# Kernel tuning notes

Hardware: AMD Instinct MI355X
Metric: run time of the kernel (lower is better)

## Reference

```python
import jax, jax.numpy as jnp
import numpy as np

N, F_IN = 4096, 128
UNITS0, HEADS0 = 16, 4   # hidden GraphAttention layer
UNITS1, HEADS1 = 1, 1    # final layer (sigmoid, mean over last axis)


def _glorot(key, shape):
    fan_in, fan_out = shape[0], shape[1]
    std = (2.0 / (fan_in + fan_out)) ** 0.5
    return std * jax.random.normal(key, shape, dtype=jnp.float32)


def setup_inputs() -> dict:
    key = jax.random.key(0)
    ks = jax.random.split(key, 8)
    x = jax.random.normal(ks[0], (N, F_IN), dtype=jnp.float32)
    adj = (jax.random.uniform(ks[1], (N, N)) < 0.01).astype(jnp.float32)
    return {
        "x": x,
        "adj": adj,
        "w0": _glorot(ks[2], (F_IN, UNITS0)),
        "aw1_0": _glorot(ks[3], (UNITS0, HEADS0)),
        "aw2_0": _glorot(ks[4], (UNITS0, HEADS0)),
        "w1": _glorot(ks[5], (UNITS0 * HEADS0, UNITS1)),
        "aw1_1": _glorot(ks[6], (UNITS1, HEADS1)),
        "aw2_1": _glorot(ks[7], (UNITS1, HEADS1)),
    }


def _gat_layer(x, adj, w, aw1, aw2, activation, final_layer):
    h = x @ w                                   # [N, units]
    a1 = h @ aw1                                # [N, H]
    a2 = h @ aw2                                # [N, H]
    # relu(a1_i + a2_j) broadcast -> [N, N, H]
    coeffs = jax.nn.relu(a1[:, None, :] + a2[None, :, :])
    # elementwise adjacency mask then softmax over neighbor axis (axis=1),
    # matching tf.nn.softmax(adj * coeffs[:,:,i], axis=1)
    attn = jax.nn.softmax(adj[:, :, None] * coeffs, axis=1)   # [N, N, H]
    # per-head aggregation then concat heads: [N, H*units]
    out = jnp.einsum('ijh,jd->ihd', attn, h).reshape(h.shape[0], -1)
    if final_layer:
        out = out.mean(axis=-1)                 # [N]
    return activation(out)


def reference(x, adj, w0, aw1_0, aw2_0, w1, aw1_1, aw2_1):
    h = _gat_layer(x, adj, w0, aw1_0, aw2_0, jax.nn.relu, False)   # [N, 64]
    out = _gat_layer(h, adj, w1, aw1_1, aw2_1, jax.nn.sigmoid, True)  # [N]
    return out
```

## Files before the change

### kernel.cpp

```cpp
#include <hip/hip_runtime.h>
#include <hip/hip_bf16.h>

#define N 4096
#define FIN 128
#define U0 16
#define H0 4
#define MAXD 128
#define NGEMM (N / 16)
#define NCSR4 (N / 4)
#define FSTRIDE 32

__global__ void k1_fused(const float* __restrict__ adj, const float* __restrict__ x,
                         const float* __restrict__ w0, const float* __restrict__ aw1,
                         const float* __restrict__ aw2,
                         int* __restrict__ deg, int* __restrict__ cols,
                         float* __restrict__ F, float* __restrict__ a1,
                         float* __restrict__ S0) {
    const int t = threadIdx.x;
    if (blockIdx.x < NGEMM) {
        const int bid = blockIdx.x;
        __shared__ float xs[16][FIN + 1];
        __shared__ float ws[FIN][U0];
        __shared__ float hs[16][U0 + 1];
        const int r0 = bid * 16;

        for (int k = t; k < FIN * U0; k += 256) ws[k / U0][k % U0] = w0[k];
        for (int k = t; k < 16 * FIN; k += 256)
            xs[k / FIN][k % FIN] = x[(size_t)(r0 + k / FIN) * FIN + (k % FIN)];
        __syncthreads();

        const int r = t / U0, u = t % U0;
        float acc = 0.f;
        #pragma unroll 8
        for (int k = 0; k < FIN; ++k) acc += xs[r][k] * ws[k][u];
        hs[r][u] = acc;
        F[(size_t)(r0 + r) * FSTRIDE + u] = acc;
        __syncthreads();

        if (t < 16 * H0) {
            const int rr = t / H0, hh = t % H0;
            float s1 = 0.f, s2 = 0.f;
            #pragma unroll
            for (int u2 = 0; u2 < U0; ++u2) {
                float hv = hs[rr][u2];
                s1 += hv * aw1[u2 * H0 + hh];
                s2 += hv * aw2[u2 * H0 + hh];
            }
            a1[(r0 + rr) * H0 + hh] = s1;
            F[(size_t)(r0 + rr) * FSTRIDE + 16 + hh] = s2;
        } else if (t >= 128 && t < 144) {
            const int d = t - 128;
            float s = 0.f;
            #pragma unroll
            for (int rr = 0; rr < 16; ++rr) s += hs[rr][d];
            atomicAdd(&S0[d], s);
        }
    } else {
        const int rb4 = (blockIdx.x - NGEMM) * 4;
        const int lane = t & 63, wid = t >> 6;

        __shared__ int cls[2][MAXD];
        __shared__ int wsum[4];
        __shared__ int dgs[2];

        for (int pair = 0; pair < 2; ++pair) {
            const int rb = rb4 + pair * 2;
            const float4* __restrict__ ar0 =
                reinterpret_cast<const float4*>(adj + (size_t)rb * N);
            const float4* __restrict__ ar1 =
                reinterpret_cast<const float4*>(adj + (size_t)(rb + 1) * N);
            float4 v0[4], v1[4];
            #pragma unroll
            for (int p = 0; p < 4; ++p) v0[p] = ar0[t + 256 * p];
            #pragma unroll
            for (int p = 0; p < 4; ++p) v1[p] = ar1[t + 256 * p];

            #pragma unroll
            for (int rr = 0; rr < 2; ++rr) {
                const float4* v = rr ? v1 : v0;
                int c = 0;
                #pragma unroll
                for (int p = 0; p < 4; ++p)
                    c += (v[p].x != 0.f) + (v[p].y != 0.f) + (v[p].z != 0.f) + (v[p].w != 0.f);

                int sc = c;
                #pragma unroll
                for (int s = 1; s < 64; s <<= 1) {
                    int u = __shfl_up(sc, s);
                    if (lane >= s) sc += u;
                }
                if (rr || pair) __syncthreads();
                if (lane == 63) wsum[wid] = sc;
                __syncthreads();
                int base = 0;
                #pragma unroll
                for (int w2 = 0; w2 < 4; ++w2)
                    if (w2 < wid) base += wsum[w2];
                const int off = base + sc - c;
                if (t == 255) dgs[rr] = min(base + sc, MAXD);

                int w = off;
                #pragma unroll
                for (int p = 0; p < 4; ++p) {
                    const int j0 = (t + 256 * p) * 4;
                    if (v[p].x != 0.f && w < MAXD) cls[rr][w++] = j0;
                    if (v[p].y != 0.f && w < MAXD) cls[rr][w++] = j0 + 1;
                    if (v[p].z != 0.f && w < MAXD) cls[rr][w++] = j0 + 2;
                    if (v[p].w != 0.f && w < MAXD) cls[rr][w++] = j0 + 3;
                }
            }
            __syncthreads();
            if (t < dgs[0]) cols[(size_t)rb * MAXD + t] = cls[0][t];
            const int t2 = t - 128;
            if (t2 >= 0 && t2 < dgs[1] && t2 < 128)
                cols[(size_t)(rb + 1) * MAXD + t2] = cls[1][t2];
            if (t < 128) {
                const int k2 = t + 128;
                if (k2 < dgs[1]) cols[(size_t)(rb + 1) * MAXD + k2] = cls[1][k2];
            }
            if (t == 0) { deg[rb] = dgs[0]; deg[rb + 1] = dgs[1]; }
        }
    }
}

__global__ void attn0(const float* __restrict__ F, const float* __restrict__ a1,
                      const float* __restrict__ S0,
                      const int* __restrict__ deg, const int* __restrict__ cols,
                      const float* __restrict__ w1, float* __restrict__ hp) {
    const int i0 = blockIdx.x * 4;
    const int t = threadIdx.x;
    __shared__ int cls[4][MAXD];

    for (int k = t; k < 4 * MAXD; k += 256) {
        const int row = k >> 7, idx = k & 127;
        const int dgr = deg[i0 + row];
        cls[row][idx] = (idx < dgr) ? cols[(size_t)(i0 + row) * MAXD + idx] : 0;
    }
    __syncthreads();

    const int w = t >> 6, lane = t & 63;
    const int i = i0 + w;
    const int dg = deg[i];
    const int q = lane >> 4, r = lane & 15;
    const int hh = r >> 2, dgc = r & 3;
    const float a1v = a1[i * H0 + hh];

    float4 accn = make_float4(0.f, 0.f, 0.f, 0.f);
    float accd = 0.f;
    for (int kb = 0; kb < dg; kb += 8) {
        const int kA = kb + q;
        const int kB = kb + 4 + q;
        const int jA = cls[w][kA < MAXD ? kA : 0];
        const int jB = cls[w][kB < MAXD ? kB : 0];
        const float msA = (kA < dg) ? 1.f : 0.f;
        const float msB = (kB < dg) ? 1.f : 0.f;
        const float* __restrict__ fA = F + (size_t)jA * FSTRIDE;
        const float* __restrict__ fB = F + (size_t)jB * FSTRIDE;
        const float4 hA = *reinterpret_cast<const float4*>(fA + dgc * 4);
        const float a2A = fA[16 + hh];
        const float4 hB = *reinterpret_cast<const float4*>(fB + dgc * 4);
        const float a2B = fB[16 + hh];

        float ccA = a1v + a2A;
        ccA = ccA > 0.f ? ccA : 0.f;
        const float eA = (__expf(ccA) - 1.f) * msA;
        accn.x = fmaf(eA, hA.x, accn.x);
        accn.y = fmaf(eA, hA.y, accn.y);
        accn.z = fmaf(eA, hA.z, accn.z);
        accn.w = fmaf(eA, hA.w, accn.w);
        accd += eA;

        float ccB = a1v + a2B;
        ccB = ccB > 0.f ? ccB : 0.f;
        const float eB = (__expf(ccB) - 1.f) * msB;
        accn.x = fmaf(eB, hB.x, accn.x);
        accn.y = fmaf(eB, hB.y, accn.y);
        accn.z = fmaf(eB, hB.z, accn.z);
        accn.w = fmaf(eB, hB.w, accn.w);
        accd += eB;
    }

    #pragma unroll
    for (int m = 16; m <= 32; m <<= 1) {
        accn.x += __shfl_xor(accn.x, m);
        accn.y += __shfl_xor(accn.y, m);
        accn.z += __shfl_xor(accn.z, m);
        accn.w += __shfl_xor(accn.w, m);
        accd   += __shfl_xor(accd, m);
    }

    const float4 s0v = reinterpret_cast<const float4*>(S0)[dgc];
    const float4 w1v = reinterpret_cast<const float4*>(w1)[r];
    const float inv = 1.f / (accd + (float)N);
    float ox = (accn.x + s0v.x) * inv; ox = ox > 0.f ? ox : 0.f;
    float oy = (accn.y + s0v.y) * inv; oy = oy > 0.f ? oy : 0.f;
    float oz = (accn.z + s0v.z) * inv; oz = oz > 0.f ? oz : 0.f;
    float ow = (accn.w + s0v.w) * inv; ow = ow > 0.f ? ow : 0.f;
    float pv = ox * w1v.x + oy * w1v.y + oz * w1v.z + ow * w1v.w;

    #pragma unroll
    for (int m = 1; m <= 8; m <<= 1) pv += __shfl_xor(pv, m);
    if (lane == 0) hp[i] = pv;
}

__global__ void attn1(const float* __restrict__ hp,
                      const float* __restrict__ aw11, const float* __restrict__ aw21,
                      const int* __restrict__ deg, const int* __restrict__ cols,
                      float* __restrict__ out) {
    __shared__ float hps[N];
    __shared__ int cls[4][MAXD];
    __shared__ float s1red[4];
    const int t = threadIdx.x;
    const int w = t >> 6, lane = t & 63;
    const int i0 = blockIdx.x * 4;

    float s = 0.f;
    const float4* __restrict__ hp4 = reinterpret_cast<const float4*>(hp);
    #pragma unroll
    for (int k = t; k < N / 4; k += 256) {
        float4 v = hp4[k];
        reinterpret_cast<float4*>(hps)[k] = v;
        s += v.x + v.y + v.z + v.w;
    }
    for (int k = t; k < 4 * MAXD; k += 256)
        cls[k >> 7][k & 127] = cols[(size_t)(i0 + (k >> 7)) * MAXD + (k & 127)];

    #pragma unroll
    for (int o = 32; o; o >>= 1) s += __shfl_down(s, o);
    if (lane == 0) s1red[w] = s;
    __syncthreads();
    const float S1 = s1red[0] + s1red[1] + s1red[2] + s1red[3];

    const int i = i0 + w;
    const float w1v = aw11[0], w2v = aw21[0];
    const float a1v = hps[i] * w1v;
    const int dg = deg[i];

    float accn = 0.f, accd = 0.f;
    for (int k = lane; k < dg; k += 64) {
        const int j = cls[w][k];
        const float hj = hps[j];
        float cc = a1v + hj * w2v;
        cc = cc > 0.f ? cc : 0.f;
        const float e = __expf(cc) - 1.f;
        accn = fmaf(e, hj, accn);
        accd += e;
    }
    #pragma unroll
    for (int o = 32; o; o >>= 1) {
        accn += __shfl_down(accn, o);
        accd += __shfl_down(accd, o);
    }
    if (lane == 0) {
        const float v = (accn + S1) / (accd + (float)N);
        out[i] = 1.f / (1.f + __expf(-v));
    }
}

extern "C" void kernel_launch(void* const* d_in, const int* in_sizes, int n_in,
                              void* d_out, int out_size, void* d_ws, size_t ws_size,
                              hipStream_t stream) {
    const float* x    = (const float*)d_in[0];
    const float* adj  = (const float*)d_in[1];
    const float* w0   = (const float*)d_in[2];
    const float* aw10 = (const float*)d_in[3];
    const float* aw20 = (const float*)d_in[4];
    const float* w1   = (const float*)d_in[5];
    const float* aw11 = (const float*)d_in[6];
    const float* aw21 = (const float*)d_in[7];
    float* out = (float*)d_out;

    char* p = (char*)d_ws;
    auto alloc = [&](size_t bytes) {
        char* r = p;
        p += (bytes + 255) & ~(size_t)255;
        return r;
    };
    float* S0   = (float*)alloc(256);
    float* F    = (float*)alloc((size_t)N * FSTRIDE * 4);
    float* a1   = (float*)alloc((size_t)N * H0 * 4);
    float* hp   = (float*)alloc((size_t)N * 4);
    int*   deg  = (int*)alloc((size_t)N * 4);
    int*   cols = (int*)alloc((size_t)N * MAXD * 4);

    hipMemsetAsync(S0, 0, 64, stream);
    k1_fused<<<NGEMM + NCSR4, 256, 0, stream>>>(adj, x, w0, aw10, aw20,
                                                deg, cols, F, a1, S0);
    attn0<<<N / 4, 256, 0, stream>>>(F, a1, S0, deg, cols, w1, hp);
    attn1<<<N / 4, 256, 0, stream>>>(hp, aw11, aw21, deg, cols, out);
}
```

Before: 34.71 us.

## Fuse attention layers into one kernel with a grid-wide flag barrier

Merges the two attention kernels into a single launch. Each block publishes a per-block flag after writing its layer-0 outputs, and every block spins until all 1024 flags are set before running layer 1. This removes one kernel launch and its drain/fill gap. In exchange it depends on all 1024 blocks being co-resident, which launch_bounds(256,4) is meant to allow across the CUs; otherwise it deadlocks. Every block also polls the flag array.

```diff
diff --git a/kernel.cpp b/kernel.cpp
--- a/kernel.cpp
+++ b/kernel.cpp
@@ -8,7 +8,9 @@
 #define MAXD 128
 #define NGEMM (N / 16)
 #define NCSR4 (N / 4)
+#define NATT  (N / 4)
 #define FSTRIDE 32
+#define SCOPE __HIP_MEMORY_SCOPE_AGENT
 
 __global__ void k1_fused(const float* __restrict__ adj, const float* __restrict__ x,
                          const float* __restrict__ w0, const float* __restrict__ aw1,
@@ -123,13 +125,21 @@
     }
 }
 
-__global__ void attn0(const float* __restrict__ F, const float* __restrict__ a1,
-                      const float* __restrict__ S0,
-                      const int* __restrict__ deg, const int* __restrict__ cols,
-                      const float* __restrict__ w1, float* __restrict__ hp) {
-    const int i0 = blockIdx.x * 4;
+__global__ __launch_bounds__(256, 4)
+void attn_mega(const float* __restrict__ F, const float* __restrict__ a1,
+               const float* __restrict__ S0,
+               const int* __restrict__ deg, const int* __restrict__ cols,
+               const float* __restrict__ w1,
+               const float* __restrict__ aw11, const float* __restrict__ aw21,
+               int* __restrict__ flagB, float* __restrict__ hp,
+               float* __restrict__ out) {
+    __shared__ int cls[4][MAXD];
+    __shared__ float hps[N];
+    __shared__ float s1red[4];
+    const int b = blockIdx.x;
+    const int i0 = b * 4;
     const int t = threadIdx.x;
-    __shared__ int cls[4][MAXD];
+    const int w = t >> 6, lane = t & 63;
 
     for (int k = t; k < 4 * MAXD; k += 256) {
         const int row = k >> 7, idx = k & 127;
@@ -138,122 +148,124 @@
     }
     __syncthreads();
 
-    const int w = t >> 6, lane = t & 63;
     const int i = i0 + w;
     const int dg = deg[i];
-    const int q = lane >> 4, r = lane & 15;
-    const int hh = r >> 2, dgc = r & 3;
-    const float a1v = a1[i * H0 + hh];
-
-    float4 accn = make_float4(0.f, 0.f, 0.f, 0.f);
-    float accd = 0.f;
-    for (int kb = 0; kb < dg; kb += 8) {
-        const int kA = kb + q;
-        const int kB = kb + 4 + q;
-        const int jA = cls[w][kA < MAXD ? kA : 0];
-        const int jB = cls[w][kB < MAXD ? kB : 0];
-        const float msA = (kA < dg) ? 1.f : 0.f;
-        const float msB = (kB < dg) ? 1.f : 0.f;
-        const float* __restrict__ fA = F + (size_t)jA * FSTRIDE;
-        const float* __restrict__ fB = F + (size_t)jB * FSTRIDE;
-        const float4 hA = *reinterpret_cast<const float4*>(fA + dgc * 4);
-        const float a2A = fA[16 + hh];
-        const float4 hB = *reinterpret_cast<const float4*>(fB + dgc * 4);
-        const float a2B = fB[16 + hh];
-
-        float ccA = a1v + a2A;
-        ccA = ccA > 0.f ? ccA : 0.f;
-        const float eA = (__expf(ccA) - 1.f) * msA;
-        accn.x = fmaf(eA, hA.x, accn.x);
-        accn.y = fmaf(eA, hA.y, accn.y);
-        accn.z = fmaf(eA, hA.z, accn.z);
-        accn.w = fmaf(eA, hA.w, accn.w);
-        accd += eA;
-
-        float ccB = a1v + a2B;
-        ccB = ccB > 0.f ? ccB : 0.f;
-        const float eB = (__expf(ccB) - 1.f) * msB;
-        accn.x = fmaf(eB, hB.x, accn.x);
-        accn.y = fmaf(eB, hB.y, accn.y);
-        accn.z = fmaf(eB, hB.z, accn.z);
-        accn.w = fmaf(eB, hB.w, accn.w);
-        accd += eB;
-    }
-
-    #pragma unroll
-    for (int m = 16; m <= 32; m <<= 1) {
-        accn.x += __shfl_xor(accn.x, m);
-        accn.y += __shfl_xor(accn.y, m);
-        accn.z += __shfl_xor(accn.z, m);
-        accn.w += __shfl_xor(accn.w, m);
-        accd   += __shfl_xor(accd, m);
-    }
-
-    const float4 s0v = reinterpret_cast<const float4*>(S0)[dgc];
-    const float4 w1v = reinterpret_cast<const float4*>(w1)[r];
-    const float inv = 1.f / (accd + (float)N);
-    float ox = (accn.x + s0v.x) * inv; ox = ox > 0.f ? ox : 0.f;
-    float oy = (accn.y + s0v.y) * inv; oy = oy > 0.f ? oy : 0.f;
-    float oz = (accn.z + s0v.z) * inv; oz = oz > 0.f ? oz : 0.f;
-    float ow = (accn.w + s0v.w) * inv; ow = ow > 0.f ? ow : 0.f;
-    float pv = ox * w1v.x + oy * w1v.y + oz * w1v.z + ow * w1v.w;
-
-    #pragma unroll
-    for (int m = 1; m <= 8; m <<= 1) pv += __shfl_xor(pv, m);
-    if (lane == 0) hp[i] = pv;
-}
-
-__global__ void attn1(const float* __restrict__ hp,
-                      const float* __restrict__ aw11, const float* __restrict__ aw21,
-                      const int* __restrict__ deg, const int* __restrict__ cols,
-                      float* __restrict__ out) {
-    __shared__ float hps[N];
-    __shared__ int cls[4][MAXD];
-    __shared__ float s1red[4];
-    const int t = threadIdx.x;
-    const int w = t >> 6, lane = t & 63;
-    const int i0 = blockIdx.x * 4;
-
-    float s = 0.f;
-    const float4* __restrict__ hp4 = reinterpret_cast<const float4*>(hp);
-    #pragma unroll
-    for (int k = t; k < N / 4; k += 256) {
-        float4 v = hp4[k];
-        reinterpret_cast<float4*>(hps)[k] = v;
-        s += v.x + v.y + v.z + v.w;
-    }
-    for (int k = t; k < 4 * MAXD; k += 256)
-        cls[k >> 7][k & 127] = cols[(size_t)(i0 + (k >> 7)) * MAXD + (k & 127)];
-
-    #pragma unroll
-    for (int o = 32; o; o >>= 1) s += __shfl_down(s, o);
-    if (lane == 0) s1red[w] = s;
+
+    {
+        const int q = lane >> 4, r = lane & 15;
+        const int hh = r >> 2, dgc = r & 3;
+        const float a1v = a1[i * H0 + hh];
+
+        float4 accn = make_float4(0.f, 0.f, 0.f, 0.f);
+        float accd = 0.f;
+        for (int kb = 0; kb < dg; kb += 8) {
+            const int kA = kb + q;
+            const int kB = kb + 4 + q;
+            const int jA = cls[w][kA < MAXD ? kA : 0];
+            const int jB = cls[w][kB < MAXD ? kB : 0];
+            const float msA = (kA < dg) ? 1.f : 0.f;
+            const float msB = (kB < dg) ? 1.f : 0.f;
+            const float* __restrict__ fA = F + (size_t)jA * FSTRIDE;
+            const float* __restrict__ fB = F + (size_t)jB * FSTRIDE;
+            const float4 hA = *reinterpret_cast<const float4*>(fA + dgc * 4);
+            const float a2A = fA[16 + hh];
+            const float4 hB = *reinterpret_cast<const float4*>(fB + dgc * 4);
+            const float a2B = fB[16 + hh];
+
+            float ccA = a1v + a2A;
+            ccA = ccA > 0.f ? ccA : 0.f;
+            const float eA = (__expf(ccA) - 1.f) * msA;
+            accn.x = fmaf(eA, hA.x, accn.x);
+            accn.y = fmaf(eA, hA.y, accn.y);
+            accn.z = fmaf(eA, hA.z, accn.z);
+            accn.w = fmaf(eA, hA.w, accn.w);
+            accd += eA;
+
+            float ccB = a1v + a2B;
+            ccB = ccB > 0.f ? ccB : 0.f;
+            const float eB = (__expf(ccB) - 1.f) * msB;
+            accn.x = fmaf(eB, hB.x, accn.x);
+            accn.y = fmaf(eB, hB.y, accn.y);
+            accn.z = fmaf(eB, hB.z, accn.z);
+            accn.w = fmaf(eB, hB.w, accn.w);
+            accd += eB;
+        }
+        #pragma unroll
+        for (int m = 16; m <= 32; m <<= 1) {
+            accn.x += __shfl_xor(accn.x, m);
+            accn.y += __shfl_xor(accn.y, m);
+            accn.z += __shfl_xor(accn.z, m);
+            accn.w += __shfl_xor(accn.w, m);
+            accd   += __shfl_xor(accd, m);
+        }
+        const float4 s0v = reinterpret_cast<const float4*>(S0)[dgc];
+        const float4 w1v = reinterpret_cast<const float4*>(w1)[r];
+        const float inv = 1.f / (accd + (float)N);
+        float ox = (accn.x + s0v.x) * inv; ox = ox > 0.f ? ox : 0.f;
+        float oy = (accn.y + s0v.y) * inv; oy = oy > 0.f ? oy : 0.f;
+        float oz = (accn.z + s0v.z) * inv; oz = oz > 0.f ? oz : 0.f;
+        float ow = (accn.w + s0v.w) * inv; ow = ow > 0.f ? ow : 0.f;
+        float pv = ox * w1v.x + oy * w1v.y + oz * w1v.z + ow * w1v.w;
+        #pragma unroll
+        for (int m = 1; m <= 8; m <<= 1) pv += __shfl_xor(pv, m);
+        if (lane == 0) hp[i] = pv;
+    }
+
     __syncthreads();
-    const float S1 = s1red[0] + s1red[1] + s1red[2] + s1red[3];
-
-    const int i = i0 + w;
-    const float w1v = aw11[0], w2v = aw21[0];
-    const float a1v = hps[i] * w1v;
-    const int dg = deg[i];
-
-    float accn = 0.f, accd = 0.f;
-    for (int k = lane; k < dg; k += 64) {
-        const int j = cls[w][k];
-        const float hj = hps[j];
-        float cc = a1v + hj * w2v;
-        cc = cc > 0.f ? cc : 0.f;
-        const float e = __expf(cc) - 1.f;
-        accn = fmaf(e, hj, accn);
-        accd += e;
-    }
-    #pragma unroll
-    for (int o = 32; o; o >>= 1) {
-        accn += __shfl_down(accn, o);
-        accd += __shfl_down(accd, o);
-    }
-    if (lane == 0) {
-        const float v = (accn + S1) / (accd + (float)N);
-        out[i] = 1.f / (1.f + __expf(-v));
+    if (t == 0) {
+        __threadfence();
+        __hip_atomic_store(&flagB[b], 1, __ATOMIC_RELEASE, SCOPE);
+    }
+    if (w == 0) {
+        for (;;) {
+            int v = 1;
+            #pragma unroll
+            for (int k = 0; k < 16; ++k)
+                v &= __hip_atomic_load(&flagB[(k << 6) | lane], __ATOMIC_RELAXED, SCOPE);
+            if (__all(v)) break;
+            __builtin_amdgcn_s_sleep(2);
+        }
+    }
+    __syncthreads();
+    if (t == 0) __threadfence();
+    __syncthreads();
+
+    {
+        float s = 0.f;
+        const float4* __restrict__ hp4 = reinterpret_cast<const float4*>(hp);
+        #pragma unroll
+        for (int k = t; k < N / 4; k += 256) {
+            float4 v = hp4[k];
+            reinterpret_cast<float4*>(hps)[k] = v;
+            s += v.x + v.y + v.z + v.w;
+        }
+        #pragma unroll
+        for (int o = 32; o; o >>= 1) s += __shfl_down(s, o);
+        if (lane == 0) s1red[w] = s;
+        __syncthreads();
+        const float S1 = s1red[0] + s1red[1] + s1red[2] + s1red[3];
+
+        const float w1s = aw11[0], w2s = aw21[0];
+        const float a1v1 = hps[i] * w1s;
+        float accn = 0.f, accd = 0.f;
+        for (int k = lane; k < dg; k += 64) {
+            const int j = cls[w][k];
+            const float hj = hps[j];
+            float cc = a1v1 + hj * w2s;
+            cc = cc > 0.f ? cc : 0.f;
+            const float e = __expf(cc) - 1.f;
+            accn = fmaf(e, hj, accn);
+            accd += e;
+        }
+        #pragma unroll
+        for (int o = 32; o; o >>= 1) {
+            accn += __shfl_down(accn, o);
+            accd += __shfl_down(accd, o);
+        }
+        if (lane == 0) {
+            const float v = (accn + S1) / (accd + (float)N);
+            out[i] = 1.f / (1.f + __expf(-v));
+        }
     }
 }
 
@@ -276,16 +288,17 @@
         p += (bytes + 255) & ~(size_t)255;
         return r;
     };
-    float* S0   = (float*)alloc(256);
-    float* F    = (float*)alloc((size_t)N * FSTRIDE * 4);
-    float* a1   = (float*)alloc((size_t)N * H0 * 4);
-    float* hp   = (float*)alloc((size_t)N * 4);
-    int*   deg  = (int*)alloc((size_t)N * 4);
-    int*   cols = (int*)alloc((size_t)N * MAXD * 4);
-
-    hipMemsetAsync(S0, 0, 64, stream);
+    float* S0    = (float*)alloc(256);
+    int*   flagB = (int*)alloc(NATT * 4);
+    float* F     = (float*)alloc((size_t)N * FSTRIDE * 4);
+    float* a1    = (float*)alloc((size_t)N * H0 * 4);
+    float* hp    = (float*)alloc((size_t)N * 4);
+    int*   deg   = (int*)alloc((size_t)N * 4);
+    int*   cols  = (int*)alloc((size_t)N * MAXD * 4);
+
+    hipMemsetAsync(S0, 0, 256 + NATT * 4, stream);
     k1_fused<<<NGEMM + NCSR4, 256, 0, stream>>>(adj, x, w0, aw10, aw20,
                                                 deg, cols, F, a1, S0);
-    attn0<<<N / 4, 256, 0, stream>>>(F, a1, S0, deg, cols, w1, hp);
-    attn1<<<N / 4, 256, 0, stream>>>(hp, aw11, aw21, deg, cols, out);
+    attn_mega<<<NATT, 256, 0, stream>>>(F, a1, S0, deg, cols, w1,
+                                        aw11, aw21, flagB, hp, out);
 }
```

Result: slower. 84.82 us (+144.4%).

## Fuse CSR build into layer-0 attention and replace atomic S0 with partial sums

Applied to the files above, without the earlier changes.

The adjacency-to-CSR compaction moves out of the first kernel and into the layer-0 attention kernel, so each block builds its four rows' neighbor lists in shared memory and uses them directly instead of reloading cols/deg from global memory. The GEMM kernel now writes per-block partial column sums of h, and every attention block reduces the 256 partials itself. This removes the memset and the atomics. The trade-off is that the 64MB adjacency scan now runs after the GEMM instead of alongside it, and each block repeats the S0 reduction.

```diff
diff --git a/kernel.cpp b/kernel.cpp
--- a/kernel.cpp
+++ b/kernel.cpp
@@ -7,140 +7,142 @@
 #define H0 4
 #define MAXD 128
 #define NGEMM (N / 16)
-#define NCSR4 (N / 4)
+#define NATT  (N / 4)
 #define FSTRIDE 32
 
-__global__ void k1_fused(const float* __restrict__ adj, const float* __restrict__ x,
-                         const float* __restrict__ w0, const float* __restrict__ aw1,
-                         const float* __restrict__ aw2,
-                         int* __restrict__ deg, int* __restrict__ cols,
-                         float* __restrict__ F, float* __restrict__ a1,
-                         float* __restrict__ S0) {
+__global__ void k1_gemm(const float* __restrict__ x, const float* __restrict__ w0,
+                        const float* __restrict__ aw1, const float* __restrict__ aw2,
+                        float* __restrict__ F, float* __restrict__ a1,
+                        float* __restrict__ partS0) {
+    __shared__ float xs[16][FIN + 1];
+    __shared__ float ws[FIN][U0];
+    __shared__ float hs[16][U0 + 1];
     const int t = threadIdx.x;
-    if (blockIdx.x < NGEMM) {
-        const int bid = blockIdx.x;
-        __shared__ float xs[16][FIN + 1];
-        __shared__ float ws[FIN][U0];
-        __shared__ float hs[16][U0 + 1];
-        const int r0 = bid * 16;
-
-        for (int k = t; k < FIN * U0; k += 256) ws[k / U0][k % U0] = w0[k];
-        for (int k = t; k < 16 * FIN; k += 256)
-            xs[k / FIN][k % FIN] = x[(size_t)(r0 + k / FIN) * FIN + (k % FIN)];
-        __syncthreads();
-
-        const int r = t / U0, u = t % U0;
-        float acc = 0.f;
-        #pragma unroll 8
-        for (int k = 0; k < FIN; ++k) acc += xs[r][k] * ws[k][u];
-        hs[r][u] = acc;
-        F[(size_t)(r0 + r) * FSTRIDE + u] = acc;
-        __syncthreads();
-
-        if (t < 16 * H0) {
-            const int rr = t / H0, hh = t % H0;
-            float s1 = 0.f, s2 = 0.f;
-            #pragma unroll
-            for (int u2 = 0; u2 < U0; ++u2) {
-                float hv = hs[rr][u2];
-                s1 += hv * aw1[u2 * H0 + hh];
-                s2 += hv * aw2[u2 * H0 + hh];
-            }
-            a1[(r0 + rr) * H0 + hh] = s1;
-            F[(size_t)(r0 + rr) * FSTRIDE + 16 + hh] = s2;
-        } else if (t >= 128 && t < 144) {
-            const int d = t - 128;
-            float s = 0.f;
-            #pragma unroll
-            for (int rr = 0; rr < 16; ++rr) s += hs[rr][d];
-            atomicAdd(&S0[d], s);
+    const int r0 = blockIdx.x * 16;
+
+    for (int k = t; k < FIN * U0; k += 256) ws[k / U0][k % U0] = w0[k];
+    for (int k = t; k < 16 * FIN; k += 256)
+        xs[k / FIN][k % FIN] = x[(size_t)(r0 + k / FIN) * FIN + (k % FIN)];
+    __syncthreads();
+
+    const int r = t / U0, u = t % U0;
+    float acc = 0.f;
+    #pragma unroll 8
+    for (int k = 0; k < FIN; ++k) acc += xs[r][k] * ws[k][u];
+    hs[r][u] = acc;
+    F[(size_t)(r0 + r) * FSTRIDE + u] = acc;
+    __syncthreads();
+
+    if (t < 16 * H0) {
+        const int rr = t / H0, hh = t % H0;
+        float s1 = 0.f, s2 = 0.f;
+        #pragma unroll
+        for (int u2 = 0; u2 < U0; ++u2) {
+            float hv = hs[rr][u2];
+            s1 += hv * aw1[u2 * H0 + hh];
+            s2 += hv * aw2[u2 * H0 + hh];
         }
-    } else {
-        const int rb4 = (blockIdx.x - NGEMM) * 4;
-        const int lane = t & 63, wid = t >> 6;
-
-        __shared__ int cls[2][MAXD];
-        __shared__ int wsum[4];
-        __shared__ int dgs[2];
-
-        for (int pair = 0; pair < 2; ++pair) {
-            const int rb = rb4 + pair * 2;
-            const float4* __restrict__ ar0 =
-                reinterpret_cast<const float4*>(adj + (size_t)rb * N);
-            const float4* __restrict__ ar1 =
-                reinterpret_cast<const float4*>(adj + (size_t)(rb + 1) * N);
-            float4 v0[4], v1[4];
-            #pragma unroll
-            for (int p = 0; p < 4; ++p) v0[p] = ar0[t + 256 * p];
-            #pragma unroll
-            for (int p = 0; p < 4; ++p) v1[p] = ar1[t + 256 * p];
-
-            #pragma unroll
-            for (int rr = 0; rr < 2; ++rr) {
-                const float4* v = rr ? v1 : v0;
-                int c = 0;
-                #pragma unroll
-                for (int p = 0; p < 4; ++p)
-                    c += (v[p].x != 0.f) + (v[p].y != 0.f) + (v[p].z != 0.f) + (v[p].w != 0.f);
-
-                int sc = c;
-                #pragma unroll
-                for (int s = 1; s < 64; s <<= 1) {
-                    int u = __shfl_up(sc, s);
-                    if (lane >= s) sc += u;
-                }
-                if (rr || pair) __syncthreads();
-                if (lane == 63) wsum[wid] = sc;
-                __syncthreads();
-                int base = 0;
-                #pragma unroll
-                for (int w2 = 0; w2 < 4; ++w2)
-                    if (w2 < wid) base += wsum[w2];
-                const int off = base + sc - c;
-                if (t == 255) dgs[rr] = min(base + sc, MAXD);
-
-                int w = off;
-                #pragma unroll
-                for (int p = 0; p < 4; ++p) {
-                    const int j0 = (t + 256 * p) * 4;
-                    if (v[p].x != 0.f && w < MAXD) cls[rr][w++] = j0;
-                    if (v[p].y != 0.f && w < MAXD) cls[rr][w++] = j0 + 1;
-                    if (v[p].z != 0.f && w < MAXD) cls[rr][w++] = j0 + 2;
-                    if (v[p].w != 0.f && w < MAXD) cls[rr][w++] = j0 + 3;
-                }
+        a1[(r0 + rr) * H0 + hh] = s1;
+        F[(size_t)(r0 + rr) * FSTRIDE + 16 + hh] = s2;
+    } else if (t >= 128 && t < 144) {
+        const int d = t - 128;
+        float s = 0.f;
+        #pragma unroll
+        for (int rr = 0; rr < 16; ++rr) s += hs[rr][d];
+        partS0[blockIdx.x * 16 + d] = s;
+    }
+}
+
+__global__ void csr_attn0(const float* __restrict__ adj, const float* __restrict__ F,
+                          const float* __restrict__ a1, const float* __restrict__ partS0,
+                          const float* __restrict__ w1,
+                          int* __restrict__ deg, int* __restrict__ cols,
+                          float* __restrict__ hp) {
+    __shared__ int   cls[4][MAXD];
+    __shared__ int   wsum[4];
+    __shared__ int   dgs[4];
+    __shared__ float red[16][17];
+    __shared__ float s0s[16];
+
+    const int t = threadIdx.x;
+    const int wid = t >> 6, lane = t & 63;
+    const int i0 = blockIdx.x * 4;
+
+    {
+        const int d = t & 15, ch = t >> 4;
+        float s = 0.f;
+        #pragma unroll
+        for (int k = ch; k < 256; k += 16) s += partS0[k * 16 + d];
+        red[ch][d] = s;
+    }
+    __syncthreads();
+    if (t < 16) {
+        float s2 = 0.f;
+        #pragma unroll
+        for (int k = 0; k < 16; ++k) s2 += red[k][t];
+        s0s[t] = s2;
+    }
+
+    for (int pair = 0; pair < 2; ++pair) {
+        const int rb = i0 + pair * 2;
+        const float4* __restrict__ ar0 =
+            reinterpret_cast<const float4*>(adj + (size_t)rb * N);
+        const float4* __restrict__ ar1 =
+            reinterpret_cast<const float4*>(adj + (size_t)(rb + 1) * N);
+        float4 v0[4], v1[4];
+        #pragma unroll
+        for (int p = 0; p < 4; ++p) v0[p] = ar0[t + 256 * p];
+        #pragma unroll
+        for (int p = 0; p < 4; ++p) v1[p] = ar1[t + 256 * p];
+
+        #pragma unroll
+        for (int rr = 0; rr < 2; ++rr) {
+            const float4* v = rr ? v1 : v0;
+            const int row = pair * 2 + rr;
+            int c = 0;
+            #pragma unroll
+            for (int p = 0; p < 4; ++p)
+                c += (v[p].x != 0.f) + (v[p].y != 0.f) + (v[p].z != 0.f) + (v[p].w != 0.f);
+
+            int sc = c;
+            #pragma unroll
+            for (int s = 1; s < 64; s <<= 1) {
+                int u = __shfl_up(sc, s);
+                if (lane >= s) sc += u;
             }
             __syncthreads();
-            if (t < dgs[0]) cols[(size_t)rb * MAXD + t] = cls[0][t];
-            const int t2 = t - 128;
-            if (t2 >= 0 && t2 < dgs[1] && t2 < 128)
-                cols[(size_t)(rb + 1) * MAXD + t2] = cls[1][t2];
-            if (t < 128) {
-                const int k2 = t + 128;
-                if (k2 < dgs[1]) cols[(size_t)(rb + 1) * MAXD + k2] = cls[1][k2];
+            if (lane == 63) wsum[wid] = sc;
+            __syncthreads();
+            int base = 0;
+            #pragma unroll
+            for (int w2 = 0; w2 < 4; ++w2)
+                if (w2 < wid) base += wsum[w2];
+            const int off = base + sc - c;
+            if (t == 255) dgs[row] = min(base + sc, MAXD);
+
+            int w = off;
+            #pragma unroll
+            for (int p = 0; p < 4; ++p) {
+                const int j0 = (t + 256 * p) * 4;
+                if (v[p].x != 0.f && w < MAXD) cls[row][w++] = j0;
+                if (v[p].y != 0.f && w < MAXD) cls[row][w++] = j0 + 1;
+                if (v[p].z != 0.f && w < MAXD) cls[row][w++] = j0 + 2;
+                if (v[p].w != 0.f && w < MAXD) cls[row][w++] = j0 + 3;
             }
-            if (t == 0) { deg[rb] = dgs[0]; deg[rb + 1] = dgs[1]; }
         }
     }
-}
-
-__global__ void attn0(const float* __restrict__ F, const float* __restrict__ a1,
-                      const float* __restrict__ S0,
-                      const int* __restrict__ deg, const int* __restrict__ cols,
-                      const float* __restrict__ w1, float* __restrict__ hp) {
-    const int i0 = blockIdx.x * 4;
-    const int t = threadIdx.x;
-    __shared__ int cls[4][MAXD];
+    __syncthreads();
 
     for (int k = t; k < 4 * MAXD; k += 256) {
         const int row = k >> 7, idx = k & 127;
-        const int dgr = deg[i0 + row];
-        cls[row][idx] = (idx < dgr) ? cols[(size_t)(i0 + row) * MAXD + idx] : 0;
-    }
-    __syncthreads();
-
-    const int w = t >> 6, lane = t & 63;
-    const int i = i0 + w;
-    const int dg = deg[i];
+        if (idx < dgs[row]) cols[(size_t)(i0 + row) * MAXD + idx] = cls[row][idx];
+        else                cls[row][idx] = 0;
+    }
+    if (t < 4) deg[i0 + t] = dgs[t];
+    __syncthreads();
+
+    const int i = i0 + wid;
+    const int dg = dgs[wid];
     const int q = lane >> 4, r = lane & 15;
     const int hh = r >> 2, dgc = r & 3;
     const float a1v = a1[i * H0 + hh];
@@ -150,8 +152,8 @@
     for (int kb = 0; kb < dg; kb += 8) {
         const int kA = kb + q;
         const int kB = kb + 4 + q;
-        const int jA = cls[w][kA < MAXD ? kA : 0];
-        const int jB = cls[w][kB < MAXD ? kB : 0];
+        const int jA = cls[wid][kA < MAXD ? kA : 0];
+        const int jB = cls[wid][kB < MAXD ? kB : 0];
         const float msA = (kA < dg) ? 1.f : 0.f;
         const float msB = (kB < dg) ? 1.f : 0.f;
         const float* __restrict__ fA = F + (size_t)jA * FSTRIDE;
@@ -179,7 +181,6 @@
         accn.w = fmaf(eB, hB.w, accn.w);
         accd += eB;
     }
-
     #pragma unroll
     for (int m = 16; m <= 32; m <<= 1) {
         accn.x += __shfl_xor(accn.x, m);
@@ -188,8 +189,7 @@
         accn.w += __shfl_xor(accn.w, m);
         accd   += __shfl_xor(accd, m);
     }
-
-    const float4 s0v = reinterpret_cast<const float4*>(S0)[dgc];
+    const float4 s0v = reinterpret_cast<const float4*>(s0s)[dgc];
     const float4 w1v = reinterpret_cast<const float4*>(w1)[r];
     const float inv = 1.f / (accd + (float)N);
     float ox = (accn.x + s0v.x) * inv; ox = ox > 0.f ? ox : 0.f;
@@ -197,7 +197,6 @@
     float oz = (accn.z + s0v.z) * inv; oz = oz > 0.f ? oz : 0.f;
     float ow = (accn.w + s0v.w) * inv; ow = ow > 0.f ? ow : 0.f;
     float pv = ox * w1v.x + oy * w1v.y + oz * w1v.z + ow * w1v.w;
-
     #pragma unroll
     for (int m = 1; m <= 8; m <<= 1) pv += __shfl_xor(pv, m);
     if (lane == 0) hp[i] = pv;
@@ -276,16 +275,14 @@
         p += (bytes + 255) & ~(size_t)255;
         return r;
     };
-    float* S0   = (float*)alloc(256);
-    float* F    = (float*)alloc((size_t)N * FSTRIDE * 4);
-    float* a1   = (float*)alloc((size_t)N * H0 * 4);
-    float* hp   = (float*)alloc((size_t)N * 4);
-    int*   deg  = (int*)alloc((size_t)N * 4);
-    int*   cols = (int*)alloc((size_t)N * MAXD * 4);
-
-    hipMemsetAsync(S0, 0, 64, stream);
-    k1_fused<<<NGEMM + NCSR4, 256, 0, stream>>>(adj, x, w0, aw10, aw20,
-                                                deg, cols, F, a1, S0);
-    attn0<<<N / 4, 256, 0, stream>>>(F, a1, S0, deg, cols, w1, hp);
-    attn1<<<N / 4, 256, 0, stream>>>(hp, aw11, aw21, deg, cols, out);
-}
+    float* partS0 = (float*)alloc(NGEMM * 16 * 4);
+    float* F      = (float*)alloc((size_t)N * FSTRIDE * 4);
+    float* a1     = (float*)alloc((size_t)N * H0 * 4);
+    float* hp     = (float*)alloc((size_t)N * 4);
+    int*   deg    = (int*)alloc((size_t)N * 4);
+    int*   cols   = (int*)alloc((size_t)N * MAXD * 4);
+
+    k1_gemm<<<NGEMM, 256, 0, stream>>>(x, w0, aw10, aw20, F, a1, partS0);
+    csr_attn0<<<NATT, 256, 0, stream>>>(adj, F, a1, partS0, w1, deg, cols, hp);
+    attn1<<<NATT, 256, 0, stream>>>(hp, aw11, aw21, deg, cols, out);
+}
```

Result: no change. 34.69 us (median of 2 runs) (-0.1%).
